# Performance work log

Hardware: AMD Instinct MI355X
Metric: run time of the kernel (lower is better)

## Reference

```python
import jax, jax.numpy as jnp
import numpy as np

B, S, H = 4, 2048, 1024
NH, HD = 16, 64
LN_EPS = 1e-5


def _l2norm(x, axis=-1, eps=1e-12):
    n = jnp.sqrt(jnp.sum(x * x, axis=axis, keepdims=True))
    return x / jnp.maximum(n, eps)


def setup_inputs() -> dict:
    key = jax.random.key(0)
    ks = jax.random.split(key, 10)
    sd = 0.02
    x = jax.random.normal(ks[0], (B, S, H), jnp.float32)
    Wq = jax.random.normal(ks[1], (H, H), jnp.float32) * sd
    Wk = jax.random.normal(ks[2], (H, H), jnp.float32) * sd
    Wv = jax.random.normal(ks[3], (H, H), jnp.float32) * sd
    Wa = jax.random.normal(ks[4], (NH, H), jnp.float32) * sd
    ba = jnp.zeros((NH,), jnp.float32)
    Wb = jax.random.normal(ks[5], (NH, H), jnp.float32) * sd
    bb = jnp.zeros((NH,), jnp.float32)
    Wg = jax.random.normal(ks[6], (H, H), jnp.float32) * sd
    Wo = jax.random.normal(ks[7], (H, H), jnp.float32) * sd
    ln_g = jnp.ones((H,), jnp.float32)
    ln_b = jnp.zeros((H,), jnp.float32)
    return {"x": x, "Wq": Wq, "Wk": Wk, "Wv": Wv, "Wa": Wa, "ba": ba,
            "Wb": Wb, "bb": bb, "Wg": Wg, "Wo": Wo, "ln_g": ln_g, "ln_b": ln_b}


def _forward(x, Wq, Wk, Wv, Wa, ba, Wb, bb, Wg, Wo, ln_g, ln_b):
    q = _l2norm((x @ Wq.T).reshape(B, S, NH, HD))  # [B,S,nh,hd]
    k = _l2norm((x @ Wk.T).reshape(B, S, NH, HD))
    v = jax.nn.silu(x @ Wv.T).reshape(B, S, NH, HD)
    alpha = jax.nn.sigmoid(x @ Wa.T + ba)  # [B,S,nh]
    beta = jax.nn.sigmoid(x @ Wb.T + bb)   # [B,S,nh]

    def step(state, inp):
        a_t, b_t, k_t, v_t, q_t = inp  # a,b: [B,nh]; k,v,q: [B,nh,hd]
        a_ = a_t[:, :, None, None]
        b_ = b_t[:, :, None, None]
        kk = k_t[..., :, None] * k_t[..., None, :]  # [B,nh,hd,hd]
        state = a_ * state * (1.0 - b_ * kk) + b_ * (v_t[..., :, None] * k_t[..., None, :])
        out_t = jnp.sum(state * q_t[..., None, :], axis=-1)  # [B,nh,hd]
        return state, out_t

    # time-major xs for scan
    xs = (jnp.moveaxis(alpha, 1, 0), jnp.moveaxis(beta, 1, 0),
          jnp.moveaxis(k, 1, 0), jnp.moveaxis(v, 1, 0), jnp.moveaxis(q, 1, 0))
    state0 = jnp.zeros((B, NH, HD, HD), x.dtype)
    _, outs = jax.lax.scan(step, state0, xs)  # [S,B,nh,hd]
    out = jnp.moveaxis(outs, 0, 1).reshape(B, S, H)

    # LayerNorm over total_dim
    mu = jnp.mean(out, axis=-1, keepdims=True)
    var = jnp.var(out, axis=-1, keepdims=True)
    out = (out - mu) / jnp.sqrt(var + LN_EPS) * ln_g + ln_b

    out = out * jax.nn.silu(x @ Wg.T)
    return out @ Wo.T


def reference(x, Wq, Wk, Wv, Wa, ba, Wb, bb, Wg, Wo, ln_g, ln_b):
    return _forward(x, Wq, Wk, Wv, Wa, ba, Wb, bb, Wg, Wo, ln_g, ln_b)
```

## Files before the change

kernel.cpp:

```cpp
#include <hip/hip_runtime.h>

typedef unsigned short u16;
typedef __bf16 bf16x8 __attribute__((ext_vector_type(8)));
typedef float f32x4 __attribute__((ext_vector_type(4)));

constexpr int Bq  = 4;
constexpr int Sq  = 2048;
constexpr int Hq  = 1024;
constexpr int NHq = 16;
constexpr int HDq = 64;
constexpr int CCH = 16;
constexpr int LCH = 128;

constexpr size_t OFF_WB = 0;
constexpr size_t OFF_XB = 10485760;
constexpr size_t OFF_Q  = 27262976;
constexpr size_t OFF_K  = 60817408;
constexpr size_t OFF_V  = 94371840;
constexpr size_t OFF_G  = 127926272;
constexpr size_t OFF_AL = 161480704;
constexpr size_t OFF_BE = 162004992;
constexpr size_t OFF_P  = 162529280;
constexpr size_t OFF_O  = 179306496;

__device__ __forceinline__ u16 f2bf(float f) {
  unsigned u = __float_as_uint(f);
  u += 0x7fffu + ((u >> 16) & 1u);
  return (u16)(u >> 16);
}
__device__ __forceinline__ float sigmoidf_(float x) { return 1.f / (1.f + __expf(-x)); }

__device__ __forceinline__ void async16(const u16* g, u16* l) {
  __builtin_amdgcn_global_load_lds((const __attribute__((address_space(1))) void*)(const void*)g,
                                   (__attribute__((address_space(3))) void*)(void*)l, 16, 0, 0);
}

__global__ __launch_bounds__(256) void cvt_x_kernel(const float* __restrict__ in, u16* __restrict__ outp) {
  const size_t i = ((size_t)blockIdx.x * 256 + threadIdx.x) * 4;
  float4 f = *(const float4*)(in + i);
  ushort4 u; u.x = f2bf(f.x); u.y = f2bf(f.y); u.z = f2bf(f.z); u.w = f2bf(f.w);
  *(ushort4*)(outp + i) = u;
}

__global__ __launch_bounds__(256) void cvt_w_kernel(const float* __restrict__ w0, const float* __restrict__ w1,
    const float* __restrict__ w2, const float* __restrict__ w3, const float* __restrict__ w4,
    u16* __restrict__ outp) {
  const int z = blockIdx.z;
  const float* src = (z == 0) ? w0 : (z == 1) ? w1 : (z == 2) ? w2 : (z == 3) ? w3 : w4;
  const size_t i = ((size_t)blockIdx.x * 256 + threadIdx.x) * 4;
  float4 f = *(const float4*)(src + i);
  ushort4 u; u.x = f2bf(f.x); u.y = f2bf(f.y); u.z = f2bf(f.z); u.w = f2bf(f.w);
  *(ushort4*)(outp + (size_t)z * (1024 * 1024) + i) = u;
}

__global__ __launch_bounds__(256) void cvt_ab_kernel(const float* __restrict__ Wa, const float* __restrict__ Wb,
    u16* __restrict__ outp) {
  const size_t i = ((size_t)blockIdx.x * 256 + threadIdx.x) * 4;
  const int row = (int)(i >> 10);
  ushort4 u;
  if (row < 32) {
    const float* src = (row < 16) ? (Wa + i) : (Wb + i - 16 * 1024);
    float4 f = *(const float4*)src;
    u.x = f2bf(f.x); u.y = f2bf(f.y); u.z = f2bf(f.z); u.w = f2bf(f.w);
  } else {
    u.x = u.y = u.z = u.w = 0;
  }
  *(ushort4*)(outp + i) = u;
}

__global__ __launch_bounds__(256) void gemm_bt(const u16* __restrict__ A, const u16* __restrict__ Wall,
    const u16* __restrict__ Wab,
    float* __restrict__ Cq, float* __restrict__ Ck, float* __restrict__ Cv, float* __restrict__ Cg,
    float* __restrict__ al, float* __restrict__ be,
    const float* __restrict__ ba, const float* __restrict__ bb, int mode) {
  constexpr int GK = 1024, GN = 1024;
  const int z = blockIdx.z;
  if (mode == 1 && z == 4 && blockIdx.y > 0) return;
  __shared__ __align__(16) u16 As[128 * 32];
  __shared__ __align__(16) u16 Bs[128 * 32];
  const int tid = threadIdx.x;
  const int w = tid >> 6, lane = tid & 63;
  const int m0 = blockIdx.x * 128, n0 = blockIdx.y * 128;
  const u16* W = (mode == 1 && z == 4) ? Wab : (Wall + (size_t)z * (1024 * 1024));
  const int rrow = lane >> 2;
  const int kc8 = (lane & 3) * 8;
  const u16* gA = A + (size_t)(m0 + w * 32 + rrow) * GK + kc8;
  const u16* gB = W + (size_t)(n0 + w * 32 + rrow) * GK + kc8;
  u16* lA = As + (w * 32) * 32;
  u16* lB = Bs + (w * 32) * 32;
  const int qd = lane >> 4, l15 = lane & 15;
  const int wm = (w >> 1) * 64, wn = (w & 1) * 64;
  f32x4 acc[4][4] = {};
  for (int kt = 0; kt < GK; kt += 32) {
    async16(gA,           lA);
    async16(gA + 16 * GK, lA + 16 * 32);
    async16(gB,           lB);
    async16(gB + 16 * GK, lB + 16 * 32);
    gA += 32; gB += 32;
    __syncthreads();
    bf16x8 af[4], bfr[4];
    #pragma unroll
    for (int i = 0; i < 4; ++i) {
      af[i]  = *(const bf16x8*)(As + (wm + i * 16 + l15) * 32 + qd * 8);
      bfr[i] = *(const bf16x8*)(Bs + (wn + i * 16 + l15) * 32 + qd * 8);
    }
    #pragma unroll
    for (int i = 0; i < 4; ++i)
      #pragma unroll
      for (int j = 0; j < 4; ++j)
        acc[i][j] = __builtin_amdgcn_mfma_f32_16x16x32_bf16(af[i], bfr[j], acc[i][j], 0, 0, 0);
    __syncthreads();
  }
  if (mode == 1 && z == 4) {
    if (wn == 0) {
      const float bav = ba[l15], bbv = bb[l15];
      #pragma unroll
      for (int i = 0; i < 4; ++i) {
        const int row = m0 + wm + i * 16 + qd * 4;
        #pragma unroll
        for (int r = 0; r < 4; ++r) {
          al[(size_t)(row + r) * 16 + l15] = sigmoidf_(acc[i][0][r] + bav);
          be[(size_t)(row + r) * 16 + l15] = sigmoidf_(acc[i][1][r] + bbv);
        }
      }
    }
    return;
  }
  if (mode == 1 && (z == 0 || z == 1)) {
    #pragma unroll
    for (int i = 0; i < 4; ++i)
      #pragma unroll
      for (int r = 0; r < 4; ++r) {
        float ss = acc[i][0][r] * acc[i][0][r] + acc[i][1][r] * acc[i][1][r]
                 + acc[i][2][r] * acc[i][2][r] + acc[i][3][r] * acc[i][3][r];
        ss += __shfl_xor(ss, 1); ss += __shfl_xor(ss, 2);
        ss += __shfl_xor(ss, 4); ss += __shfl_xor(ss, 8);
        const float rn = 1.f / fmaxf(sqrtf(ss), 1e-12f);
        acc[i][0][r] *= rn; acc[i][1][r] *= rn; acc[i][2][r] *= rn; acc[i][3][r] *= rn;
      }
  } else if (mode == 1 && z == 2) {
    #pragma unroll
    for (int i = 0; i < 4; ++i)
      #pragma unroll
      for (int j = 0; j < 4; ++j)
        #pragma unroll
        for (int r = 0; r < 4; ++r)
          acc[i][j][r] = acc[i][j][r] * sigmoidf_(acc[i][j][r]);
  }
  float* C = (mode == 0) ? Cq : ((z == 0) ? Cq : (z == 1) ? Ck : (z == 2) ? Cv : Cg);
  #pragma unroll
  for (int i = 0; i < 4; ++i) {
    const int row = m0 + wm + i * 16 + qd * 4;
    #pragma unroll
    for (int j = 0; j < 4; ++j) {
      const int col = n0 + wn + j * 16 + l15;
      #pragma unroll
      for (int r = 0; r < 4; ++r)
        C[(size_t)(row + r) * GN + col] = acc[i][j][r];
    }
  }
}

struct S1 { float4 kc0, kc1, kr0, kr1, vr0, vr1; float a, bt; };
struct S2 { float4 kc0, kc1, qc0, qc1, kr0, kr1, vr0, vr1; float a, bt; };

__device__ __forceinline__ void load_s1(const float* __restrict__ k, const float* __restrict__ v,
    const float* __restrict__ al, const float* __restrict__ be,
    size_t base, size_t ab, int c8, int r8, S1& s) {
  s.kc0 = *(const float4*)(k + base + c8);     s.kc1 = *(const float4*)(k + base + c8 + 4);
  s.kr0 = *(const float4*)(k + base + r8);     s.kr1 = *(const float4*)(k + base + r8 + 4);
  s.vr0 = *(const float4*)(v + base + r8);     s.vr1 = *(const float4*)(v + base + r8 + 4);
  s.a = al[ab]; s.bt = be[ab];
}

__device__ __forceinline__ void load_s2(const float* __restrict__ q, const float* __restrict__ k,
    const float* __restrict__ v, const float* __restrict__ al, const float* __restrict__ be,
    size_t base, size_t ab, int c8, int r8, S2& s) {
  s.kc0 = *(const float4*)(k + base + c8);     s.kc1 = *(const float4*)(k + base + c8 + 4);
  s.qc0 = *(const float4*)(q + base + c8);     s.qc1 = *(const float4*)(q + base + c8 + 4);
  s.kr0 = *(const float4*)(k + base + r8);     s.kr1 = *(const float4*)(k + base + r8 + 4);
  s.vr0 = *(const float4*)(v + base + r8);     s.vr1 = *(const float4*)(v + base + r8 + 4);
  s.a = al[ab]; s.bt = be[ab];
}

__global__ __launch_bounds__(256) void scan_p1(const float* __restrict__ k, const float* __restrict__ v,
    const float* __restrict__ al, const float* __restrict__ be,
    float* __restrict__ P, float* __restrict__ Q) {
  const int w = threadIdx.x >> 6, lane = threadIdx.x & 63;
  const int g = blockIdx.x * 4 + w;
  const int c = g & 15;
  const int bh = g >> 4;
  const int b = bh >> 4, h = bh & 15;
  const int r8 = (lane >> 3) * 8, c8 = (lane & 7) * 8;
  const int t0 = c * LCH;
  const size_t base0 = ((size_t)(b * Sq + t0)) * 1024 + h * 64;
  const size_t ab0   = ((size_t)(b * Sq + t0)) * 16 + h;
  float Pr[64], Qr[64];
  #pragma unroll
  for (int i = 0; i < 64; ++i) { Pr[i] = 1.f; Qr[i] = 0.f; }
  S1 buf[2];
  load_s1(k, v, al, be, base0,        ab0,      c8, r8, buf[0]);
  load_s1(k, v, al, be, base0 + 1024, ab0 + 16, c8, r8, buf[1]);
  for (int tb = 0; tb < LCH; tb += 2) {
    #pragma unroll
    for (int d = 0; d < 2; ++d) {
      const S1 s = buf[d];
      const int tn = tb + d + 2;
      load_s1(k, v, al, be, base0 + (size_t)tn * 1024, ab0 + (size_t)tn * 16, c8, r8, buf[d]);
      const float kcv[8] = {s.kc0.x, s.kc0.y, s.kc0.z, s.kc0.w, s.kc1.x, s.kc1.y, s.kc1.z, s.kc1.w};
      const float krv[8] = {s.kr0.x, s.kr0.y, s.kr0.z, s.kr0.w, s.kr1.x, s.kr1.y, s.kr1.z, s.kr1.w};
      const float vrv[8] = {s.vr0.x, s.vr0.y, s.vr0.z, s.vr0.w, s.vr1.x, s.vr1.y, s.vr1.z, s.vr1.w};
      const float abt = s.a * s.bt;
      float c1[8], c2[8];
      #pragma unroll
      for (int i = 0; i < 8; ++i) { c1[i] = abt * krv[i]; c2[i] = s.bt * vrv[i]; }
      #pragma unroll
      for (int i = 0; i < 8; ++i)
        #pragma unroll
        for (int j = 0; j < 8; ++j) {
          const int e = i * 8 + j;
          const float A = fmaf(-c1[i], kcv[j], s.a);
          Qr[e] = fmaf(A, Qr[e], c2[i] * kcv[j]);
          Pr[e] *= A;
        }
    }
  }
  const size_t pbase = ((size_t)bh * CCH + c) * 4096 + (size_t)c8;
  #pragma unroll
  for (int i = 0; i < 8; ++i) {
    const size_t pi = pbase + (size_t)(r8 + i) * 64;
    *(float4*)(P + pi)     = make_float4(Pr[i*8],   Pr[i*8+1], Pr[i*8+2], Pr[i*8+3]);
    *(float4*)(P + pi + 4) = make_float4(Pr[i*8+4], Pr[i*8+5], Pr[i*8+6], Pr[i*8+7]);
    *(float4*)(Q + pi)     = make_float4(Qr[i*8],   Qr[i*8+1], Qr[i*8+2], Qr[i*8+3]);
    *(float4*)(Q + pi + 4) = make_float4(Qr[i*8+4], Qr[i*8+5], Qr[i*8+6], Qr[i*8+7]);
  }
}

__global__ __launch_bounds__(256) void scan_comb(float* __restrict__ P, const float* __restrict__ Q) {
  const int g = blockIdx.x * 256 + threadIdx.x;
  const int elem = g & 4095;
  const int bh = g >> 12;
  float s = 0.f;
  for (int c = 0; c < CCH; ++c) {
    const size_t idx = ((size_t)bh * CCH + c) * 4096 + elem;
    const float p = P[idx], qq = Q[idx];
    P[idx] = s;
    s = fmaf(p, s, qq);
  }
}

__global__ __launch_bounds__(256) void scan_p2(const float* __restrict__ q, const float* __restrict__ k,
    const float* __restrict__ v, const float* __restrict__ al, const float* __restrict__ be,
    const float* __restrict__ Pini, float* __restrict__ o) {
  const int w = threadIdx.x >> 6, lane = threadIdx.x & 63;
  const int g = blockIdx.x * 4 + w;
  const int c = g & 15;
  const int bh = g >> 4;
  const int b = bh >> 4, h = bh & 15;
  const int cb = lane & 7;
  const int r8 = (lane >> 3) * 8, c8 = cb * 8;
  const int t0 = c * LCH;
  const size_t base0 = ((size_t)(b * Sq + t0)) * 1024 + h * 64;
  const size_t ab0   = ((size_t)(b * Sq + t0)) * 16 + h;
  const size_t pbase = ((size_t)bh * CCH + c) * 4096 + (size_t)c8;
  float st[64];
  #pragma unroll
  for (int i = 0; i < 8; ++i) {
    float4 s0 = *(const float4*)(Pini + pbase + (size_t)(r8 + i) * 64);
    float4 s1 = *(const float4*)(Pini + pbase + (size_t)(r8 + i) * 64 + 4);
    st[i*8]   = s0.x; st[i*8+1] = s0.y; st[i*8+2] = s0.z; st[i*8+3] = s0.w;
    st[i*8+4] = s1.x; st[i*8+5] = s1.y; st[i*8+6] = s1.z; st[i*8+7] = s1.w;
  }
  S2 buf[2];
  load_s2(q, k, v, al, be, base0,        ab0,      c8, r8, buf[0]);
  load_s2(q, k, v, al, be, base0 + 1024, ab0 + 16, c8, r8, buf[1]);
  const bool hi4 = (cb & 4), hi2 = (cb & 2), hi1 = (cb & 1);
  for (int tb = 0; tb < LCH; tb += 2) {
    #pragma unroll
    for (int d = 0; d < 2; ++d) {
      const int t = tb + d;
      const S2 s = buf[d];
      const int tn = t + 2;
      load_s2(q, k, v, al, be, base0 + (size_t)tn * 1024, ab0 + (size_t)tn * 16, c8, r8, buf[d]);
      const float kcv[8] = {s.kc0.x, s.kc0.y, s.kc0.z, s.kc0.w, s.kc1.x, s.kc1.y, s.kc1.z, s.kc1.w};
      const float qcv[8] = {s.qc0.x, s.qc0.y, s.qc0.z, s.qc0.w, s.qc1.x, s.qc1.y, s.qc1.z, s.qc1.w};
      const float krv[8] = {s.kr0.x, s.kr0.y, s.kr0.z, s.kr0.w, s.kr1.x, s.kr1.y, s.kr1.z, s.kr1.w};
      const float vrv[8] = {s.vr0.x, s.vr0.y, s.vr0.z, s.vr0.w, s.vr1.x, s.vr1.y, s.vr1.z, s.vr1.w};
      const float abt = s.a * s.bt;
      float c1[8], c2[8];
      #pragma unroll
      for (int i = 0; i < 8; ++i) { c1[i] = abt * krv[i]; c2[i] = s.bt * vrv[i]; }
      float p[8];
      #pragma unroll
      for (int i = 0; i < 8; ++i) p[i] = 0.f;
      #pragma unroll
      for (int i = 0; i < 8; ++i)
        #pragma unroll
        for (int j = 0; j < 8; ++j) {
          const int e = i * 8 + j;
          const float A = fmaf(-c1[i], kcv[j], s.a);
          st[e] = fmaf(A, st[e], c2[i] * kcv[j]);
          p[i] = fmaf(st[e], qcv[j], p[i]);
        }
      float r4[4];
      #pragma unroll
      for (int i = 0; i < 4; ++i) {
        const float send = hi4 ? p[i] : p[i + 4];
        const float recv = __shfl_xor(send, 4);
        r4[i] = (hi4 ? p[i + 4] : p[i]) + recv;
      }
      float r2[2];
      #pragma unroll
      for (int i = 0; i < 2; ++i) {
        const float send = hi2 ? r4[i] : r4[i + 2];
        const float recv = __shfl_xor(send, 2);
        r2[i] = (hi2 ? r4[i + 2] : r4[i]) + recv;
      }
      {
        const float send = hi1 ? r2[0] : r2[1];
        const float recv = __shfl_xor(send, 1);
        const float tot = (hi1 ? r2[1] : r2[0]) + recv;
        o[base0 + (size_t)t * 1024 + lane] = tot;
      }
    }
  }
}

__global__ __launch_bounds__(256) void ln_gate_kernel(const float* __restrict__ o, const float* __restrict__ g,
    const float* __restrict__ ln_g, const float* __restrict__ ln_b, u16* __restrict__ y) {
  const int t = blockIdx.x, tid = threadIdx.x;
  const size_t row = (size_t)t * 1024;
  float4 xv = *(const float4*)(o + row + tid * 4);
  float s  = xv.x + xv.y + xv.z + xv.w;
  float s2 = xv.x * xv.x + xv.y * xv.y + xv.z * xv.z + xv.w * xv.w;
  #pragma unroll
  for (int m = 1; m < 64; m <<= 1) { s += __shfl_xor(s, m); s2 += __shfl_xor(s2, m); }
  __shared__ float red[8];
  const int w = tid >> 6, lane = tid & 63;
  if (lane == 0) { red[w] = s; red[4 + w] = s2; }
  __syncthreads();
  s  = red[0] + red[1] + red[2] + red[3];
  s2 = red[4] + red[5] + red[6] + red[7];
  const float mu = s * (1.f / 1024.f);
  const float var = s2 * (1.f / 1024.f) - mu * mu;
  const float rstd = rsqrtf(var + 1e-5f);
  float4 gv = *(const float4*)(g + row + tid * 4);
  float4 lg = *(const float4*)(ln_g + tid * 4);
  float4 lb = *(const float4*)(ln_b + tid * 4);
  ushort4 u;
  u.x = f2bf(((xv.x - mu) * rstd * lg.x + lb.x) * (gv.x * sigmoidf_(gv.x)));
  u.y = f2bf(((xv.y - mu) * rstd * lg.y + lb.y) * (gv.y * sigmoidf_(gv.y)));
  u.z = f2bf(((xv.z - mu) * rstd * lg.z + lb.z) * (gv.z * sigmoidf_(gv.z)));
  u.w = f2bf(((xv.w - mu) * rstd * lg.w + lb.w) * (gv.w * sigmoidf_(gv.w)));
  *(ushort4*)(y + row + tid * 4) = u;
}

extern "C" void kernel_launch(void* const* d_in, const int* in_sizes, int n_in,
                              void* d_out, int out_size, void* d_ws, size_t ws_size,
                              hipStream_t stream) {
  const float* x    = (const float*)d_in[0];
  const float* Wq   = (const float*)d_in[1];
  const float* Wk   = (const float*)d_in[2];
  const float* Wv   = (const float*)d_in[3];
  const float* Wa   = (const float*)d_in[4];
  const float* ba   = (const float*)d_in[5];
  const float* Wb   = (const float*)d_in[6];
  const float* bb   = (const float*)d_in[7];
  const float* Wg   = (const float*)d_in[8];
  const float* Wo   = (const float*)d_in[9];
  const float* ln_g = (const float*)d_in[10];
  const float* ln_b = (const float*)d_in[11];
  float* out = (float*)d_out;
  char* ws = (char*)d_ws;

  u16*   wb  = (u16*)(ws + OFF_WB);
  u16*   xb  = (u16*)(ws + OFF_XB);
  float* qf  = (float*)(ws + OFF_Q);
  float* kf  = (float*)(ws + OFF_K);
  float* vf  = (float*)(ws + OFF_V);
  float* gf  = (float*)(ws + OFF_G);
  float* al  = (float*)(ws + OFF_AL);
  float* be  = (float*)(ws + OFF_BE);
  u16*   wab = (u16*)(ws + OFF_P);
  float* Pb  = (float*)(ws + OFF_P);
  float* Qc  = (float*)(ws + OFF_XB);
  float* of  = (float*)(ws + OFF_O);
  u16*   yb  = xb;

  cvt_x_kernel<<<8192, 256, 0, stream>>>(x, xb);
  cvt_w_kernel<<<dim3(1024, 1, 5), 256, 0, stream>>>(Wq, Wk, Wv, Wg, Wo, wb);
  cvt_ab_kernel<<<128, 256, 0, stream>>>(Wa, Wb, wab);
  gemm_bt<<<dim3(64, 8, 5), 256, 0, stream>>>(xb, wb, wab, qf, kf, vf, gf, al, be, ba, bb, 1);
  scan_p1<<<256, 256, 0, stream>>>(kf, vf, al, be, Pb, Qc);
  scan_comb<<<1024, 256, 0, stream>>>(Pb, Qc);
  scan_p2<<<256, 256, 0, stream>>>(qf, kf, vf, al, be, Pb, of);
  ln_gate_kernel<<<8192, 256, 0, stream>>>(of, gf, ln_g, ln_b, yb);
  gemm_bt<<<dim3(64, 8, 1), 256, 0, stream>>>(yb, wb + (size_t)4 * 1024 * 1024, wab,
                                              out, out, out, out, al, be, ba, bb, 0);
}
```

Before: 453.7 us.

## Split each scan chunk's 64x64 state across two waves and deepen prefetch

```diff
diff --git a/kernel.cpp b/kernel.cpp
--- a/kernel.cpp
+++ b/kernel.cpp
@@ -161,61 +161,65 @@
   }
 }
 
-struct S1 { float4 kc0, kc1, kr0, kr1, vr0, vr1; float a, bt; };
-struct S2 { float4 kc0, kc1, qc0, qc1, kr0, kr1, vr0, vr1; float a, bt; };
-
-__device__ __forceinline__ void load_s1(const float* __restrict__ k, const float* __restrict__ v,
+
+struct S1h { float4 kc0, kc1, kr, vr; float a, bt; };
+struct S2h { float4 kc0, kc1, qc0, qc1, kr, vr; float a, bt; };
+
+__device__ __forceinline__ void load_s1h(const float* __restrict__ k, const float* __restrict__ v,
     const float* __restrict__ al, const float* __restrict__ be,
-    size_t base, size_t ab, int c8, int r8, S1& s) {
-  s.kc0 = *(const float4*)(k + base + c8);     s.kc1 = *(const float4*)(k + base + c8 + 4);
-  s.kr0 = *(const float4*)(k + base + r8);     s.kr1 = *(const float4*)(k + base + r8 + 4);
-  s.vr0 = *(const float4*)(v + base + r8);     s.vr1 = *(const float4*)(v + base + r8 + 4);
+    size_t base, size_t ab, int c8, int r0, S1h& s) {
+  s.kc0 = *(const float4*)(k + base + c8);  s.kc1 = *(const float4*)(k + base + c8 + 4);
+  s.kr  = *(const float4*)(k + base + r0);
+  s.vr  = *(const float4*)(v + base + r0);
   s.a = al[ab]; s.bt = be[ab];
 }
 
-__device__ __forceinline__ void load_s2(const float* __restrict__ q, const float* __restrict__ k,
+__device__ __forceinline__ void load_s2h(const float* __restrict__ q, const float* __restrict__ k,
     const float* __restrict__ v, const float* __restrict__ al, const float* __restrict__ be,
-    size_t base, size_t ab, int c8, int r8, S2& s) {
-  s.kc0 = *(const float4*)(k + base + c8);     s.kc1 = *(const float4*)(k + base + c8 + 4);
-  s.qc0 = *(const float4*)(q + base + c8);     s.qc1 = *(const float4*)(q + base + c8 + 4);
-  s.kr0 = *(const float4*)(k + base + r8);     s.kr1 = *(const float4*)(k + base + r8 + 4);
-  s.vr0 = *(const float4*)(v + base + r8);     s.vr1 = *(const float4*)(v + base + r8 + 4);
+    size_t base, size_t ab, int c8, int r0, S2h& s) {
+  s.kc0 = *(const float4*)(k + base + c8);  s.kc1 = *(const float4*)(k + base + c8 + 4);
+  s.qc0 = *(const float4*)(q + base + c8);  s.qc1 = *(const float4*)(q + base + c8 + 4);
+  s.kr  = *(const float4*)(k + base + r0);
+  s.vr  = *(const float4*)(v + base + r0);
   s.a = al[ab]; s.bt = be[ab];
 }
 
-__global__ __launch_bounds__(256) void scan_p1(const float* __restrict__ k, const float* __restrict__ v,
+__global__ __launch_bounds__(256, 2) void scan_p1(const float* __restrict__ k, const float* __restrict__ v,
     const float* __restrict__ al, const float* __restrict__ be,
     float* __restrict__ P, float* __restrict__ Q) {
   const int w = threadIdx.x >> 6, lane = threadIdx.x & 63;
-  const int g = blockIdx.x * 4 + w;
-  const int c = g & 15;
-  const int bh = g >> 4;
+  const int gw = blockIdx.x * 4 + w;
+  const int half = gw & 1;
+  const int c = (gw >> 1) & 15;
+  const int bh = gw >> 5;
   const int b = bh >> 4, h = bh & 15;
-  const int r8 = (lane >> 3) * 8, c8 = (lane & 7) * 8;
+  const int rg = lane >> 3, cg = lane & 7;
+  const int r0 = half * 32 + rg * 4, c8 = cg * 8;
   const int t0 = c * LCH;
   const size_t base0 = ((size_t)(b * Sq + t0)) * 1024 + h * 64;
   const size_t ab0   = ((size_t)(b * Sq + t0)) * 16 + h;
-  float Pr[64], Qr[64];
-  #pragma unroll
-  for (int i = 0; i < 64; ++i) { Pr[i] = 1.f; Qr[i] = 0.f; }
-  S1 buf[2];
-  load_s1(k, v, al, be, base0,        ab0,      c8, r8, buf[0]);
-  load_s1(k, v, al, be, base0 + 1024, ab0 + 16, c8, r8, buf[1]);
-  for (int tb = 0; tb < LCH; tb += 2) {
-    #pragma unroll
-    for (int d = 0; d < 2; ++d) {
-      const S1 s = buf[d];
-      const int tn = tb + d + 2;
-      load_s1(k, v, al, be, base0 + (size_t)tn * 1024, ab0 + (size_t)tn * 16, c8, r8, buf[d]);
+  float Pr[32], Qr[32];
+  #pragma unroll
+  for (int i = 0; i < 32; ++i) { Pr[i] = 1.f; Qr[i] = 0.f; }
+  S1h buf[4];
+  #pragma unroll
+  for (int d = 0; d < 4; ++d)
+    load_s1h(k, v, al, be, base0 + (size_t)d * 1024, ab0 + (size_t)d * 16, c8, r0, buf[d]);
+  for (int tb = 0; tb < LCH; tb += 4) {
+    #pragma unroll
+    for (int d = 0; d < 4; ++d) {
+      const S1h s = buf[d];
+      const int tn = tb + d + 4;
+      load_s1h(k, v, al, be, base0 + (size_t)tn * 1024, ab0 + (size_t)tn * 16, c8, r0, buf[d]);
       const float kcv[8] = {s.kc0.x, s.kc0.y, s.kc0.z, s.kc0.w, s.kc1.x, s.kc1.y, s.kc1.z, s.kc1.w};
-      const float krv[8] = {s.kr0.x, s.kr0.y, s.kr0.z, s.kr0.w, s.kr1.x, s.kr1.y, s.kr1.z, s.kr1.w};
-      const float vrv[8] = {s.vr0.x, s.vr0.y, s.vr0.z, s.vr0.w, s.vr1.x, s.vr1.y, s.vr1.z, s.vr1.w};
+      const float krv[4] = {s.kr.x, s.kr.y, s.kr.z, s.kr.w};
+      const float vrv[4] = {s.vr.x, s.vr.y, s.vr.z, s.vr.w};
       const float abt = s.a * s.bt;
-      float c1[8], c2[8];
-      #pragma unroll
-      for (int i = 0; i < 8; ++i) { c1[i] = abt * krv[i]; c2[i] = s.bt * vrv[i]; }
-      #pragma unroll
-      for (int i = 0; i < 8; ++i)
+      float c1[4], c2[4];
+      #pragma unroll
+      for (int i = 0; i < 4; ++i) { c1[i] = abt * krv[i]; c2[i] = s.bt * vrv[i]; }
+      #pragma unroll
+      for (int i = 0; i < 4; ++i)
         #pragma unroll
         for (int j = 0; j < 8; ++j) {
           const int e = i * 8 + j;
@@ -227,11 +231,11 @@
   }
   const size_t pbase = ((size_t)bh * CCH + c) * 4096 + (size_t)c8;
   #pragma unroll
-  for (int i = 0; i < 8; ++i) {
-    const size_t pi = pbase + (size_t)(r8 + i) * 64;
-    *(float4*)(P + pi)     = make_float4(Pr[i*8],   Pr[i*8+1], Pr[i*8+2], Pr[i*8+3]);
+  for (int i = 0; i < 4; ++i) {
+    const size_t pi = pbase + (size_t)(r0 + i) * 64;
+    *(float4*)(P + pi) = make_float4(Pr[i*8],   Pr[i*8+1], Pr[i*8+2], Pr[i*8+3]);
     *(float4*)(P + pi + 4) = make_float4(Pr[i*8+4], Pr[i*8+5], Pr[i*8+6], Pr[i*8+7]);
-    *(float4*)(Q + pi)     = make_float4(Qr[i*8],   Qr[i*8+1], Qr[i*8+2], Qr[i*8+3]);
+    *(float4*)(Q + pi) = make_float4(Qr[i*8],   Qr[i*8+1], Qr[i*8+2], Qr[i*8+3]);
     *(float4*)(Q + pi + 4) = make_float4(Qr[i*8+4], Qr[i*8+5], Qr[i*8+6], Qr[i*8+7]);
   }
 }
@@ -249,52 +253,56 @@
   }
 }
 
-__global__ __launch_bounds__(256) void scan_p2(const float* __restrict__ q, const float* __restrict__ k,
+__global__ __launch_bounds__(256, 2) void scan_p2(const float* __restrict__ q, const float* __restrict__ k,
     const float* __restrict__ v, const float* __restrict__ al, const float* __restrict__ be,
     const float* __restrict__ Pini, float* __restrict__ o) {
   const int w = threadIdx.x >> 6, lane = threadIdx.x & 63;
-  const int g = blockIdx.x * 4 + w;
-  const int c = g & 15;
-  const int bh = g >> 4;
+  const int gw = blockIdx.x * 4 + w;
+  const int half = gw & 1;
+  const int c = (gw >> 1) & 15;
+  const int bh = gw >> 5;
   const int b = bh >> 4, h = bh & 15;
-  const int cb = lane & 7;
-  const int r8 = (lane >> 3) * 8, c8 = cb * 8;
+  const int rg = lane >> 3, cg = lane & 7;
+  const int r0 = half * 32 + rg * 4, c8 = cg * 8;
   const int t0 = c * LCH;
   const size_t base0 = ((size_t)(b * Sq + t0)) * 1024 + h * 64;
   const size_t ab0   = ((size_t)(b * Sq + t0)) * 16 + h;
   const size_t pbase = ((size_t)bh * CCH + c) * 4096 + (size_t)c8;
-  float st[64];
-  #pragma unroll
-  for (int i = 0; i < 8; ++i) {
-    float4 s0 = *(const float4*)(Pini + pbase + (size_t)(r8 + i) * 64);
-    float4 s1 = *(const float4*)(Pini + pbase + (size_t)(r8 + i) * 64 + 4);
+  float st[32];
+  #pragma unroll
+  for (int i = 0; i < 4; ++i) {
+    float4 s0 = *(const float4*)(Pini + pbase + (size_t)(r0 + i) * 64);
+    float4 s1 = *(const float4*)(Pini + pbase + (size_t)(r0 + i) * 64 + 4);
     st[i*8]   = s0.x; st[i*8+1] = s0.y; st[i*8+2] = s0.z; st[i*8+3] = s0.w;
     st[i*8+4] = s1.x; st[i*8+5] = s1.y; st[i*8+6] = s1.z; st[i*8+7] = s1.w;
   }
-  S2 buf[2];
-  load_s2(q, k, v, al, be, base0,        ab0,      c8, r8, buf[0]);
-  load_s2(q, k, v, al, be, base0 + 1024, ab0 + 16, c8, r8, buf[1]);
-  const bool hi4 = (cb & 4), hi2 = (cb & 2), hi1 = (cb & 1);
-  for (int tb = 0; tb < LCH; tb += 2) {
-    #pragma unroll
-    for (int d = 0; d < 2; ++d) {
+  S2h buf[4];
+  #pragma unroll
+  for (int d = 0; d < 4; ++d)
+    load_s2h(q, k, v, al, be, base0 + (size_t)d * 1024, ab0 + (size_t)d * 16, c8, r0, buf[d]);
+  const bool hi4 = (cg & 4), hi2 = (cg & 2);
+  const int rowIdx = r0 + (cg >> 1);
+  const bool doStore = ((cg & 1) == 0);
+  for (int tb = 0; tb < LCH; tb += 4) {
+    #pragma unroll
+    for (int d = 0; d < 4; ++d) {
       const int t = tb + d;
-      const S2 s = buf[d];
-      const int tn = t + 2;
-      load_s2(q, k, v, al, be, base0 + (size_t)tn * 1024, ab0 + (size_t)tn * 16, c8, r8, buf[d]);
+      const S2h s = buf[d];
+      const int tn = t + 4;
+      load_s2h(q, k, v, al, be, base0 + (size_t)tn * 1024, ab0 + (size_t)tn * 16, c8, r0, buf[d]);
       const float kcv[8] = {s.kc0.x, s.kc0.y, s.kc0.z, s.kc0.w, s.kc1.x, s.kc1.y, s.kc1.z, s.kc1.w};
       const float qcv[8] = {s.qc0.x, s.qc0.y, s.qc0.z, s.qc0.w, s.qc1.x, s.qc1.y, s.qc1.z, s.qc1.w};
-      const float krv[8] = {s.kr0.x, s.kr0.y, s.kr0.z, s.kr0.w, s.kr1.x, s.kr1.y, s.kr1.z, s.kr1.w};
-      const float vrv[8] = {s.vr0.x, s.vr0.y, s.vr0.z, s.vr0.w, s.vr1.x, s.vr1.y, s.vr1.z, s.vr1.w};
+      const float krv[4] = {s.kr.x, s.kr.y, s.kr.z, s.kr.w};
+      const float vrv[4] = {s.vr.x, s.vr.y, s.vr.z, s.vr.w};
       const float abt = s.a * s.bt;
-      float c1[8], c2[8];
-      #pragma unroll
-      for (int i = 0; i < 8; ++i) { c1[i] = abt * krv[i]; c2[i] = s.bt * vrv[i]; }
-      float p[8];
-      #pragma unroll
-      for (int i = 0; i < 8; ++i) p[i] = 0.f;
-      #pragma unroll
-      for (int i = 0; i < 8; ++i)
+      float c1[4], c2[4];
+      #pragma unroll
+      for (int i = 0; i < 4; ++i) { c1[i] = abt * krv[i]; c2[i] = s.bt * vrv[i]; }
+      float p[4];
+      #pragma unroll
+      for (int i = 0; i < 4; ++i) p[i] = 0.f;
+      #pragma unroll
+      for (int i = 0; i < 4; ++i)
         #pragma unroll
         for (int j = 0; j < 8; ++j) {
           const int e = i * 8 + j;
@@ -302,26 +310,21 @@
           st[e] = fmaf(A, st[e], c2[i] * kcv[j]);
           p[i] = fmaf(st[e], qcv[j], p[i]);
         }
-      float r4[4];
-      #pragma unroll
-      for (int i = 0; i < 4; ++i) {
-        const float send = hi4 ? p[i] : p[i + 4];
+      float r2[2];
+      #pragma unroll
+      for (int i = 0; i < 2; ++i) {
+        const float send = hi4 ? p[i] : p[i + 2];
         const float recv = __shfl_xor(send, 4);
-        r4[i] = (hi4 ? p[i + 4] : p[i]) + recv;
+        r2[i] = (hi4 ? p[i + 2] : p[i]) + recv;
       }
-      float r2[2];
-      #pragma unroll
-      for (int i = 0; i < 2; ++i) {
-        const float send = hi2 ? r4[i] : r4[i + 2];
+      float r1;
+      {
+        const float send = hi2 ? r2[0] : r2[1];
         const float recv = __shfl_xor(send, 2);
-        r2[i] = (hi2 ? r4[i + 2] : r4[i]) + recv;
+        r1 = (hi2 ? r2[1] : r2[0]) + recv;
       }
-      {
-        const float send = hi1 ? r2[0] : r2[1];
-        const float recv = __shfl_xor(send, 1);
-        const float tot = (hi1 ? r2[1] : r2[0]) + recv;
-        o[base0 + (size_t)t * 1024 + lane] = tot;
-      }
+      const float tot = r1 + __shfl_xor(r1, 1);
+      if (doStore) o[base0 + (size_t)t * 1024 + rowIdx] = tot;
     }
   }
 }
@@ -391,9 +394,9 @@
   cvt_w_kernel<<<dim3(1024, 1, 5), 256, 0, stream>>>(Wq, Wk, Wv, Wg, Wo, wb);
   cvt_ab_kernel<<<128, 256, 0, stream>>>(Wa, Wb, wab);
   gemm_bt<<<dim3(64, 8, 5), 256, 0, stream>>>(xb, wb, wab, qf, kf, vf, gf, al, be, ba, bb, 1);
-  scan_p1<<<256, 256, 0, stream>>>(kf, vf, al, be, Pb, Qc);
+  scan_p1<<<512, 256, 0, stream>>>(kf, vf, al, be, Pb, Qc);
   scan_comb<<<1024, 256, 0, stream>>>(Pb, Qc);
-  scan_p2<<<256, 256, 0, stream>>>(qf, kf, vf, al, be, Pb, of);
+  scan_p2<<<512, 256, 0, stream>>>(qf, kf, vf, al, be, Pb, of);
   ln_gate_kernel<<<8192, 256, 0, stream>>>(of, gf, ln_g, ln_b, yb);
   gemm_bt<<<dim3(64, 8, 1), 256, 0, stream>>>(yb, wb + (size_t)4 * 1024 * 1024, wab,
                                               out, out, out, out, al, be, ba, bb, 0);
```

Result: slower. 493.9 us (+8.9%).

## Stage scan inputs through double-buffered LDS with async global-to-LDS loads

Applied to the files above, without the earlier changes.

```diff
diff --git a/kernel.cpp b/kernel.cpp
--- a/kernel.cpp
+++ b/kernel.cpp
@@ -30,9 +30,9 @@
 }
 __device__ __forceinline__ float sigmoidf_(float x) { return 1.f / (1.f + __expf(-x)); }
 
-__device__ __forceinline__ void async16(const u16* g, u16* l) {
-  __builtin_amdgcn_global_load_lds((const __attribute__((address_space(1))) void*)(const void*)g,
-                                   (__attribute__((address_space(3))) void*)(void*)l, 16, 0, 0);
+__device__ __forceinline__ void async16(const void* g, void* l) {
+  __builtin_amdgcn_global_load_lds((const __attribute__((address_space(1))) void*)g,
+                                   (__attribute__((address_space(3))) void*)l, 16, 0, 0);
 }
 
 __global__ __launch_bounds__(256) void cvt_x_kernel(const float* __restrict__ in, u16* __restrict__ outp) {
@@ -161,65 +161,67 @@
   }
 }
 
-struct S1 { float4 kc0, kc1, kr0, kr1, vr0, vr1; float a, bt; };
-struct S2 { float4 kc0, kc1, qc0, qc1, kr0, kr1, vr0, vr1; float a, bt; };
-
-__device__ __forceinline__ void load_s1(const float* __restrict__ k, const float* __restrict__ v,
-    const float* __restrict__ al, const float* __restrict__ be,
-    size_t base, size_t ab, int c8, int r8, S1& s) {
-  s.kc0 = *(const float4*)(k + base + c8);     s.kc1 = *(const float4*)(k + base + c8 + 4);
-  s.kr0 = *(const float4*)(k + base + r8);     s.kr1 = *(const float4*)(k + base + r8 + 4);
-  s.vr0 = *(const float4*)(v + base + r8);     s.vr1 = *(const float4*)(v + base + r8 + 4);
-  s.a = al[ab]; s.bt = be[ab];
-}
-
-__device__ __forceinline__ void load_s2(const float* __restrict__ q, const float* __restrict__ k,
-    const float* __restrict__ v, const float* __restrict__ al, const float* __restrict__ be,
-    size_t base, size_t ab, int c8, int r8, S2& s) {
-  s.kc0 = *(const float4*)(k + base + c8);     s.kc1 = *(const float4*)(k + base + c8 + 4);
-  s.qc0 = *(const float4*)(q + base + c8);     s.qc1 = *(const float4*)(q + base + c8 + 4);
-  s.kr0 = *(const float4*)(k + base + r8);     s.kr1 = *(const float4*)(k + base + r8 + 4);
-  s.vr0 = *(const float4*)(v + base + r8);     s.vr1 = *(const float4*)(v + base + r8 + 4);
-  s.a = al[ab]; s.bt = be[ab];
-}
+struct ScanLds1 { float kb[2][4][16 * 64]; float vb[2][4][16 * 64]; float ab[2][4][32]; };
+struct ScanLds2 { float kb[2][4][16 * 64]; float qb[2][4][16 * 64]; float vb[2][4][16 * 64]; float ab[2][4][32]; };
 
 __global__ __launch_bounds__(256) void scan_p1(const float* __restrict__ k, const float* __restrict__ v,
     const float* __restrict__ al, const float* __restrict__ be,
     float* __restrict__ P, float* __restrict__ Q) {
-  const int w = threadIdx.x >> 6, lane = threadIdx.x & 63;
-  const int g = blockIdx.x * 4 + w;
-  const int c = g & 15;
-  const int bh = g >> 4;
+  __shared__ ScanLds1 L;
+  const int tid = threadIdx.x, wv = tid >> 6, lane = tid & 63;
+  const int bh = blockIdx.x >> 2;
+  const int c = (blockIdx.x & 3) * 4 + wv;
   const int b = bh >> 4, h = bh & 15;
   const int r8 = (lane >> 3) * 8, c8 = (lane & 7) * 8;
-  const int t0 = c * LCH;
-  const size_t base0 = ((size_t)(b * Sq + t0)) * 1024 + h * 64;
-  const size_t ab0   = ((size_t)(b * Sq + t0)) * 16 + h;
+  const size_t base0 = ((size_t)(b * Sq + c * LCH)) * 1024 + h * 64;
+  const size_t ab0   = ((size_t)(b * Sq + c * LCH)) * 16 + h;
+  const int tokw = lane >> 4, seg = lane & 15;
+  auto stage = [&](int tile, int bi) {
+    const size_t tb = base0 + (size_t)tile * 16 * 1024;
+    #pragma unroll
+    for (int i = 0; i < 4; ++i) {
+      async16(k + tb + (size_t)(i * 4 + tokw) * 1024 + seg * 4, &L.kb[bi][wv][i * 256]);
+      async16(v + tb + (size_t)(i * 4 + tokw) * 1024 + seg * 4, &L.vb[bi][wv][i * 256]);
+    }
+    if (lane < 32) {
+      const float* src = (lane < 16) ? al : be;
+      const int tt = lane & 15;
+      L.ab[bi][wv][(lane < 16 ? 0 : 16) + tt] = src[ab0 + (size_t)(tile * 16 + tt) * 16];
+    }
+  };
   float Pr[64], Qr[64];
   #pragma unroll
   for (int i = 0; i < 64; ++i) { Pr[i] = 1.f; Qr[i] = 0.f; }
-  S1 buf[2];
-  load_s1(k, v, al, be, base0,        ab0,      c8, r8, buf[0]);
-  load_s1(k, v, al, be, base0 + 1024, ab0 + 16, c8, r8, buf[1]);
-  for (int tb = 0; tb < LCH; tb += 2) {
-    #pragma unroll
-    for (int d = 0; d < 2; ++d) {
-      const S1 s = buf[d];
-      const int tn = tb + d + 2;
-      load_s1(k, v, al, be, base0 + (size_t)tn * 1024, ab0 + (size_t)tn * 16, c8, r8, buf[d]);
-      const float kcv[8] = {s.kc0.x, s.kc0.y, s.kc0.z, s.kc0.w, s.kc1.x, s.kc1.y, s.kc1.z, s.kc1.w};
-      const float krv[8] = {s.kr0.x, s.kr0.y, s.kr0.z, s.kr0.w, s.kr1.x, s.kr1.y, s.kr1.z, s.kr1.w};
-      const float vrv[8] = {s.vr0.x, s.vr0.y, s.vr0.z, s.vr0.w, s.vr1.x, s.vr1.y, s.vr1.z, s.vr1.w};
-      const float abt = s.a * s.bt;
+  stage(0, 0);
+  for (int tile = 0; tile < 8; ++tile) {
+    __syncthreads();
+    if (tile < 7) stage(tile + 1, (tile + 1) & 1);
+    const int bi = tile & 1;
+    const float* kbp = L.kb[bi][wv];
+    const float* vbp = L.vb[bi][wv];
+    const float* abp = L.ab[bi][wv];
+    #pragma unroll 2
+    for (int tt = 0; tt < 16; ++tt) {
+      const float a = abp[tt], bt = abp[16 + tt];
+      float4 kcv0 = *(const float4*)(kbp + tt * 64 + c8);
+      float4 kcv1 = *(const float4*)(kbp + tt * 64 + c8 + 4);
+      float4 krv0 = *(const float4*)(kbp + tt * 64 + r8);
+      float4 krv1 = *(const float4*)(kbp + tt * 64 + r8 + 4);
+      float4 vrv0 = *(const float4*)(vbp + tt * 64 + r8);
+      float4 vrv1 = *(const float4*)(vbp + tt * 64 + r8 + 4);
+      const float kcv[8] = {kcv0.x, kcv0.y, kcv0.z, kcv0.w, kcv1.x, kcv1.y, kcv1.z, kcv1.w};
+      const float krv[8] = {krv0.x, krv0.y, krv0.z, krv0.w, krv1.x, krv1.y, krv1.z, krv1.w};
+      const float vrv[8] = {vrv0.x, vrv0.y, vrv0.z, vrv0.w, vrv1.x, vrv1.y, vrv1.z, vrv1.w};
+      const float abt = a * bt;
       float c1[8], c2[8];
       #pragma unroll
-      for (int i = 0; i < 8; ++i) { c1[i] = abt * krv[i]; c2[i] = s.bt * vrv[i]; }
+      for (int i = 0; i < 8; ++i) { c1[i] = abt * krv[i]; c2[i] = bt * vrv[i]; }
       #pragma unroll
       for (int i = 0; i < 8; ++i)
         #pragma unroll
         for (int j = 0; j < 8; ++j) {
           const int e = i * 8 + j;
-          const float A = fmaf(-c1[i], kcv[j], s.a);
+          const float A = fmaf(-c1[i], kcv[j], a);
           Qr[e] = fmaf(A, Qr[e], c2[i] * kcv[j]);
           Pr[e] *= A;
         }
@@ -252,17 +254,31 @@
 __global__ __launch_bounds__(256) void scan_p2(const float* __restrict__ q, const float* __restrict__ k,
     const float* __restrict__ v, const float* __restrict__ al, const float* __restrict__ be,
     const float* __restrict__ Pini, float* __restrict__ o) {
-  const int w = threadIdx.x >> 6, lane = threadIdx.x & 63;
-  const int g = blockIdx.x * 4 + w;
-  const int c = g & 15;
-  const int bh = g >> 4;
+  __shared__ ScanLds2 L;
+  const int tid = threadIdx.x, wv = tid >> 6, lane = tid & 63;
+  const int bh = blockIdx.x >> 2;
+  const int c = (blockIdx.x & 3) * 4 + wv;
   const int b = bh >> 4, h = bh & 15;
   const int cb = lane & 7;
   const int r8 = (lane >> 3) * 8, c8 = cb * 8;
-  const int t0 = c * LCH;
-  const size_t base0 = ((size_t)(b * Sq + t0)) * 1024 + h * 64;
-  const size_t ab0   = ((size_t)(b * Sq + t0)) * 16 + h;
+  const size_t base0 = ((size_t)(b * Sq + c * LCH)) * 1024 + h * 64;
+  const size_t ab0   = ((size_t)(b * Sq + c * LCH)) * 16 + h;
   const size_t pbase = ((size_t)bh * CCH + c) * 4096 + (size_t)c8;
+  const int tokw = lane >> 4, seg = lane & 15;
+  auto stage = [&](int tile, int bi) {
+    const size_t tb = base0 + (size_t)tile * 16 * 1024;
+    #pragma unroll
+    for (int i = 0; i < 4; ++i) {
+      async16(k + tb + (size_t)(i * 4 + tokw) * 1024 + seg * 4, &L.kb[bi][wv][i * 256]);
+      async16(q + tb + (size_t)(i * 4 + tokw) * 1024 + seg * 4, &L.qb[bi][wv][i * 256]);
+      async16(v + tb + (size_t)(i * 4 + tokw) * 1024 + seg * 4, &L.vb[bi][wv][i * 256]);
+    }
+    if (lane < 32) {
+      const float* src = (lane < 16) ? al : be;
+      const int tt = lane & 15;
+      L.ab[bi][wv][(lane < 16 ? 0 : 16) + tt] = src[ab0 + (size_t)(tile * 16 + tt) * 16];
+    }
+  };
   float st[64];
   #pragma unroll
   for (int i = 0; i < 8; ++i) {
@@ -271,25 +287,36 @@
     st[i*8]   = s0.x; st[i*8+1] = s0.y; st[i*8+2] = s0.z; st[i*8+3] = s0.w;
     st[i*8+4] = s1.x; st[i*8+5] = s1.y; st[i*8+6] = s1.z; st[i*8+7] = s1.w;
   }
-  S2 buf[2];
-  load_s2(q, k, v, al, be, base0,        ab0,      c8, r8, buf[0]);
-  load_s2(q, k, v, al, be, base0 + 1024, ab0 + 16, c8, r8, buf[1]);
+  stage(0, 0);
   const bool hi4 = (cb & 4), hi2 = (cb & 2), hi1 = (cb & 1);
-  for (int tb = 0; tb < LCH; tb += 2) {
-    #pragma unroll
-    for (int d = 0; d < 2; ++d) {
-      const int t = tb + d;
-      const S2 s = buf[d];
-      const int tn = t + 2;
-      load_s2(q, k, v, al, be, base0 + (size_t)tn * 1024, ab0 + (size_t)tn * 16, c8, r8, buf[d]);
-      const float kcv[8] = {s.kc0.x, s.kc0.y, s.kc0.z, s.kc0.w, s.kc1.x, s.kc1.y, s.kc1.z, s.kc1.w};
-      const float qcv[8] = {s.qc0.x, s.qc0.y, s.qc0.z, s.qc0.w, s.qc1.x, s.qc1.y, s.qc1.z, s.qc1.w};
-      const float krv[8] = {s.kr0.x, s.kr0.y, s.kr0.z, s.kr0.w, s.kr1.x, s.kr1.y, s.kr1.z, s.kr1.w};
-      const float vrv[8] = {s.vr0.x, s.vr0.y, s.vr0.z, s.vr0.w, s.vr1.x, s.vr1.y, s.vr1.z, s.vr1.w};
-      const float abt = s.a * s.bt;
+  for (int tile = 0; tile < 8; ++tile) {
+    __syncthreads();
+    if (tile < 7) stage(tile + 1, (tile + 1) & 1);
+    const int bi = tile & 1;
+    const float* kbp = L.kb[bi][wv];
+    const float* qbp = L.qb[bi][wv];
+    const float* vbp = L.vb[bi][wv];
+    const float* abp = L.ab[bi][wv];
+    #pragma unroll 2
+    for (int tt = 0; tt < 16; ++tt) {
+      const int t = tile * 16 + tt;
+      const float a = abp[tt], bt = abp[16 + tt];
+      float4 kcv0 = *(const float4*)(kbp + tt * 64 + c8);
+      float4 kcv1 = *(const float4*)(kbp + tt * 64 + c8 + 4);
+      float4 qcv0 = *(const float4*)(qbp + tt * 64 + c8);
+      float4 qcv1 = *(const float4*)(qbp + tt * 64 + c8 + 4);
+      float4 krv0 = *(const float4*)(kbp + tt * 64 + r8);
+      float4 krv1 = *(const float4*)(kbp + tt * 64 + r8 + 4);
+      float4 vrv0 = *(const float4*)(vbp + tt * 64 + r8);
+      float4 vrv1 = *(const float4*)(vbp + tt * 64 + r8 + 4);
+      const float kcv[8] = {kcv0.x, kcv0.y, kcv0.z, kcv0.w, kcv1.x, kcv1.y, kcv1.z, kcv1.w};
+      const float qcv[8] = {qcv0.x, qcv0.y, qcv0.z, qcv0.w, qcv1.x, qcv1.y, qcv1.z, qcv1.w};
+      const float krv[8] = {krv0.x, krv0.y, krv0.z, krv0.w, krv1.x, krv1.y, krv1.z, krv1.w};
+      const float vrv[8] = {vrv0.x, vrv0.y, vrv0.z, vrv0.w, vrv1.x, vrv1.y, vrv1.z, vrv1.w};
+      const float abt = a * bt;
       float c1[8], c2[8];
       #pragma unroll
-      for (int i = 0; i < 8; ++i) { c1[i] = abt * krv[i]; c2[i] = s.bt * vrv[i]; }
+      for (int i = 0; i < 8; ++i) { c1[i] = abt * krv[i]; c2[i] = bt * vrv[i]; }
       float p[8];
       #pragma unroll
       for (int i = 0; i < 8; ++i) p[i] = 0.f;
@@ -298,7 +325,7 @@
         #pragma unroll
         for (int j = 0; j < 8; ++j) {
           const int e = i * 8 + j;
-          const float A = fmaf(-c1[i], kcv[j], s.a);
+          const float A = fmaf(-c1[i], kcv[j], a);
           st[e] = fmaf(A, st[e], c2[i] * kcv[j]);
           p[i] = fmaf(st[e], qcv[j], p[i]);
         }
```

Measured after the change: 454.6 us. About the same (+0.2%).
